# Optimization experiments

Hardware: AMD Instinct MI355X
Metric: run time of the kernel (lower is better)

Reference implementation:

```python
import jax, jax.numpy as jnp
import numpy as np

NUM_HEADS = 16
D_K = 8          # = n_wires in _QLayer
EMBED_DIM = NUM_HEADS * D_K
BATCH, SEQ = 8, 1024


def quantum_heads(x, theta):
    """Exact analytic simulation of the per-head 8-qubit circuit.

    Circuit per head vector v (len 8): RX(v_i) encoding on wire i, then
    trainable RX(theta_i) on wire i (RX angles add on |0>), then CNOT chain
    (0->1),(1->2),...,(6->7),(7->0), then <PauliZ> on every wire.

    Before the CNOTs each qubit is cos(a/2)|0> - i sin(a/2)|1> with
    a_i = v_i + theta_i, so bit_i ~ Bernoulli(sin^2(a_i/2)) independently and
    E[(-1)^{bit_i}] = cos(a_i). The CNOT chain is a permutation of basis
    states acting linearly over GF(2): output bit w is the XOR of input bits
    dep(w), where dep(0) = {1..7} and dep(w) = {0..w} for w>=1. Hence
    <Z_w> = prod_{j in dep(w)} cos(a_j).
    """
    b, s, e = x.shape
    a = x.reshape(b, s, NUM_HEADS, D_K) + theta      # [b,s,h,8]
    c = jnp.cos(a)
    cp = jnp.cumprod(c, axis=-1)                     # prefix products c0..cw
    z0 = jnp.prod(c[..., 1:], axis=-1, keepdims=True)  # wire 0: cos(a1)...cos(a7)
    z = jnp.concatenate([z0, cp[..., 1:]], axis=-1)  # [b,s,h,8]
    return z.reshape(b, s, e)


def setup_inputs() -> dict:
    key = jax.random.key(0)
    k1, k2, k3 = jax.random.split(key, 3)
    x = jax.random.normal(k1, (BATCH, SEQ, EMBED_DIM), dtype=jnp.float32)
    theta = jax.random.normal(k2, (D_K,), dtype=jnp.float32)
    w_combine = jax.random.normal(k3, (EMBED_DIM, EMBED_DIM), dtype=jnp.float32) * 0.05
    return {"x": x, "theta": theta, "w_combine": w_combine}


def reference(x, theta, w_combine):
    b, s, e = x.shape
    # The module calls the SAME _QLayer on the same x three times, so q=k=v.
    meas = quantum_heads(x, theta)                                   # [b,s,e]
    qkv = meas.reshape(b, s, NUM_HEADS, D_K).transpose(0, 2, 1, 3)   # [b,h,s,d]
    scores = jnp.einsum('bhqd,bhkd->bhqk', qkv, qkv) / np.float32(np.sqrt(D_K))
    attn = jax.nn.softmax(scores, axis=-1)
    out = jnp.einsum('bhqk,bhkd->bhqd', attn, qkv)
    out = out.transpose(0, 2, 1, 3).reshape(b, s, e)
    return out @ w_combine.T  # bias-free combine_heads Linear
```

## Files before the change

kernel.cpp:

```cpp
#include <hip/hip_runtime.h>
#include <hip/hip_bf16.h>

#define NUM_HEADS 16
#define EMBED 128
#define BATCH 8
#define SEQ 1024
#define ROWS (BATCH*SEQ)
#define QSCALE 0.5101256830f

#if __has_builtin(__builtin_amdgcn_exp2f)
#define EXP2(x) __builtin_amdgcn_exp2f(x)
#else
#define EXP2(x) exp2f(x)
#endif

__global__ __launch_bounds__(256) void k_wt(const float* __restrict__ w,
                                            float* __restrict__ wt) {
    int idx = blockIdx.x * 256 + threadIdx.x;
    int e = idx >> 7;
    int f = idx & 127;
    wt[f * 128 + e] = w[idx];
}

__global__ __launch_bounds__(256) void k_attn(const float* __restrict__ x,
                                              const float* __restrict__ theta,
                                              float* __restrict__ attn) {
    __shared__ __align__(16) float z[SEQ * 8];
    const int bid = blockIdx.x;
    const int bh = bid >> 1, qh = bid & 1;
    const int b = bh >> 4, h = bh & 15;
    const int t = threadIdx.x;

    float th[8];
#pragma unroll
    for (int i = 0; i < 8; ++i) th[i] = theta[i];

    float q[2][8];
#pragma unroll
    for (int j = 0; j < 4; ++j) {
        int r = t + 256 * j;
        const float* xp = x + ((size_t)((b << 10) + r)) * 128 + h * 8;
        float4 a0 = *(const float4*)xp;
        float4 a1 = *(const float4*)(xp + 4);
        float c0 = cosf(a0.x + th[0]);
        float c1 = cosf(a0.y + th[1]);
        float c2 = cosf(a0.z + th[2]);
        float c3 = cosf(a0.w + th[3]);
        float c4 = cosf(a1.x + th[4]);
        float c5 = cosf(a1.y + th[5]);
        float c6 = cosf(a1.z + th[6]);
        float c7 = cosf(a1.w + th[7]);
        float z1 = c0 * c1;
        float z2 = z1 * c2;
        float z3 = z2 * c3;
        float z4 = z3 * c4;
        float z5 = z4 * c5;
        float z6 = z5 * c6;
        float z7 = z6 * c7;
        float z0 = c1 * c2;
        z0 *= c3; z0 *= c4; z0 *= c5; z0 *= c6; z0 *= c7;
        *(float4*)&z[r * 8]     = make_float4(z0, z1, z2, z3);
        *(float4*)&z[r * 8 + 4] = make_float4(z4, z5, z6, z7);
        if ((j >> 1) == qh) {
            int jj = j & 1;
            q[jj][0] = z0 * QSCALE; q[jj][1] = z1 * QSCALE;
            q[jj][2] = z2 * QSCALE; q[jj][3] = z3 * QSCALE;
            q[jj][4] = z4 * QSCALE; q[jj][5] = z5 * QSCALE;
            q[jj][6] = z6 * QSCALE; q[jj][7] = z7 * QSCALE;
        }
    }
    __syncthreads();

    float o[2][8];
#pragma unroll
    for (int jj = 0; jj < 2; ++jj)
#pragma unroll
        for (int i = 0; i < 8; ++i) o[jj][i] = 0.f;
    float sm0 = 0.f, sm1 = 0.f;

#pragma unroll 4
    for (int kk = 0; kk < SEQ; ++kk) {
        float4 k0 = *(const float4*)&z[kk * 8];
        float4 k1 = *(const float4*)&z[kk * 8 + 4];
        float s0 = q[0][0]*k0.x + q[0][1]*k0.y + q[0][2]*k0.z + q[0][3]*k0.w
                 + q[0][4]*k1.x + q[0][5]*k1.y + q[0][6]*k1.z + q[0][7]*k1.w;
        float s1 = q[1][0]*k0.x + q[1][1]*k0.y + q[1][2]*k0.z + q[1][3]*k0.w
                 + q[1][4]*k1.x + q[1][5]*k1.y + q[1][6]*k1.z + q[1][7]*k1.w;
        float p0 = EXP2(s0);
        float p1 = EXP2(s1);
        sm0 += p0; sm1 += p1;
        o[0][0] += p0*k0.x; o[0][1] += p0*k0.y; o[0][2] += p0*k0.z; o[0][3] += p0*k0.w;
        o[0][4] += p0*k1.x; o[0][5] += p0*k1.y; o[0][6] += p0*k1.z; o[0][7] += p0*k1.w;
        o[1][0] += p1*k0.x; o[1][1] += p1*k0.y; o[1][2] += p1*k0.z; o[1][3] += p1*k0.w;
        o[1][4] += p1*k1.x; o[1][5] += p1*k1.y; o[1][6] += p1*k1.z; o[1][7] += p1*k1.w;
    }

    float inv0 = 1.0f / sm0;
    float inv1 = 1.0f / sm1;
    int r0 = qh * 512 + t;
    float* op = attn + ((size_t)((b << 10) + r0)) * 128 + h * 8;
    *(float4*)op       = make_float4(o[0][0]*inv0, o[0][1]*inv0, o[0][2]*inv0, o[0][3]*inv0);
    *(float4*)(op + 4) = make_float4(o[0][4]*inv0, o[0][5]*inv0, o[0][6]*inv0, o[0][7]*inv0);
    op += (size_t)256 * 128;
    *(float4*)op       = make_float4(o[1][0]*inv1, o[1][1]*inv1, o[1][2]*inv1, o[1][3]*inv1);
    *(float4*)(op + 4) = make_float4(o[1][4]*inv1, o[1][5]*inv1, o[1][6]*inv1, o[1][7]*inv1);
}

__global__ __launch_bounds__(256) void k_combine(const float* __restrict__ a,
                                                 const float* __restrict__ wt,
                                                 float* __restrict__ out) {
    int t = threadIdx.x;
    int e = t & 127;
    int half = t >> 7;
    size_t r0 = (size_t)blockIdx.x * 8 + half * 4;
    const float* arow = a + r0 * 128;

    float acc0 = 0.f, acc1 = 0.f, acc2 = 0.f, acc3 = 0.f;
#pragma unroll 4
    for (int f = 0; f < 128; ++f) {
        float wv = wt[f * 128 + e];
        acc0 += arow[f]       * wv;
        acc1 += arow[128 + f] * wv;
        acc2 += arow[256 + f] * wv;
        acc3 += arow[384 + f] * wv;
    }
    out[(r0 + 0) * 128 + e] = acc0;
    out[(r0 + 1) * 128 + e] = acc1;
    out[(r0 + 2) * 128 + e] = acc2;
    out[(r0 + 3) * 128 + e] = acc3;
}

extern "C" void kernel_launch(void* const* d_in, const int* in_sizes, int n_in,
                              void* d_out, int out_size, void* d_ws, size_t ws_size,
                              hipStream_t stream) {
    const float* x     = (const float*)d_in[0];
    const float* theta = (const float*)d_in[1];
    const float* w     = (const float*)d_in[2];
    float* out = (float*)d_out;

    float* attn = (float*)d_ws;
    float* wt   = (float*)((char*)d_ws + (size_t)ROWS * EMBED * 4);

    k_wt<<<64, 256, 0, stream>>>(w, wt);
    k_attn<<<256, 256, 0, stream>>>(x, theta, attn);
    k_combine<<<ROWS / 8, 256, 0, stream>>>(attn, wt, out);
}
```

Measured before the change: 165.3 us.

## Split attention queries across more blocks and stage combine rows in LDS

The attention kernel now launches 512 blocks, each handling 256 query rows with one query per thread instead of two. This doubles parallelism on the many-CU GPU, at the cost of recomputing the shared K/V (cosine products) in twice as many blocks. The combine kernel stages 16 activation rows in shared memory and computes 8 rows per thread with float4 LDS reads, reusing each weight load across more rows. It also adds FMA intrinsics, inline v_exp_f32 and launch-bounds occupancy hints.

```diff
diff --git a/kernel.cpp b/kernel.cpp
--- a/kernel.cpp
+++ b/kernel.cpp
@@ -8,11 +8,11 @@
 #define ROWS (BATCH*SEQ)
 #define QSCALE 0.5101256830f
 
-#if __has_builtin(__builtin_amdgcn_exp2f)
-#define EXP2(x) __builtin_amdgcn_exp2f(x)
-#else
-#define EXP2(x) exp2f(x)
-#endif
+__device__ __forceinline__ float fast_exp2(float x) {
+    float r;
+    asm("v_exp_f32 %0, %1" : "=v"(r) : "v"(x));
+    return r;
+}
 
 __global__ __launch_bounds__(256) void k_wt(const float* __restrict__ w,
                                             float* __restrict__ wt) {
@@ -22,12 +22,12 @@
     wt[f * 128 + e] = w[idx];
 }
 
-__global__ __launch_bounds__(256) void k_attn(const float* __restrict__ x,
-                                              const float* __restrict__ theta,
-                                              float* __restrict__ attn) {
+__global__ __launch_bounds__(256, 2) void k_attn(const float* __restrict__ x,
+                                                 const float* __restrict__ theta,
+                                                 float* __restrict__ attn) {
     __shared__ __align__(16) float z[SEQ * 8];
     const int bid = blockIdx.x;
-    const int bh = bid >> 1, qh = bid & 1;
+    const int bh = bid >> 2, qc = bid & 3;
     const int b = bh >> 4, h = bh & 15;
     const int t = threadIdx.x;
 
@@ -35,7 +35,7 @@
 #pragma unroll
     for (int i = 0; i < 8; ++i) th[i] = theta[i];
 
-    float q[2][8];
+    float q[8];
 #pragma unroll
     for (int j = 0; j < 4; ++j) {
         int r = t + 256 * j;
@@ -61,73 +61,88 @@
         z0 *= c3; z0 *= c4; z0 *= c5; z0 *= c6; z0 *= c7;
         *(float4*)&z[r * 8]     = make_float4(z0, z1, z2, z3);
         *(float4*)&z[r * 8 + 4] = make_float4(z4, z5, z6, z7);
-        if ((j >> 1) == qh) {
-            int jj = j & 1;
-            q[jj][0] = z0 * QSCALE; q[jj][1] = z1 * QSCALE;
-            q[jj][2] = z2 * QSCALE; q[jj][3] = z3 * QSCALE;
-            q[jj][4] = z4 * QSCALE; q[jj][5] = z5 * QSCALE;
-            q[jj][6] = z6 * QSCALE; q[jj][7] = z7 * QSCALE;
+        if (j == qc) {
+            q[0] = z0 * QSCALE; q[1] = z1 * QSCALE;
+            q[2] = z2 * QSCALE; q[3] = z3 * QSCALE;
+            q[4] = z4 * QSCALE; q[5] = z5 * QSCALE;
+            q[6] = z6 * QSCALE; q[7] = z7 * QSCALE;
         }
     }
     __syncthreads();
 
-    float o[2][8];
-#pragma unroll
-    for (int jj = 0; jj < 2; ++jj)
-#pragma unroll
-        for (int i = 0; i < 8; ++i) o[jj][i] = 0.f;
-    float sm0 = 0.f, sm1 = 0.f;
+    float o0 = 0.f, o1 = 0.f, o2 = 0.f, o3 = 0.f;
+    float o4 = 0.f, o5 = 0.f, o6 = 0.f, o7 = 0.f;
+    float sm = 0.f;
 
 #pragma unroll 4
     for (int kk = 0; kk < SEQ; ++kk) {
         float4 k0 = *(const float4*)&z[kk * 8];
         float4 k1 = *(const float4*)&z[kk * 8 + 4];
-        float s0 = q[0][0]*k0.x + q[0][1]*k0.y + q[0][2]*k0.z + q[0][3]*k0.w
-                 + q[0][4]*k1.x + q[0][5]*k1.y + q[0][6]*k1.z + q[0][7]*k1.w;
-        float s1 = q[1][0]*k0.x + q[1][1]*k0.y + q[1][2]*k0.z + q[1][3]*k0.w
-                 + q[1][4]*k1.x + q[1][5]*k1.y + q[1][6]*k1.z + q[1][7]*k1.w;
-        float p0 = EXP2(s0);
-        float p1 = EXP2(s1);
-        sm0 += p0; sm1 += p1;
-        o[0][0] += p0*k0.x; o[0][1] += p0*k0.y; o[0][2] += p0*k0.z; o[0][3] += p0*k0.w;
-        o[0][4] += p0*k1.x; o[0][5] += p0*k1.y; o[0][6] += p0*k1.z; o[0][7] += p0*k1.w;
-        o[1][0] += p1*k0.x; o[1][1] += p1*k0.y; o[1][2] += p1*k0.z; o[1][3] += p1*k0.w;
-        o[1][4] += p1*k1.x; o[1][5] += p1*k1.y; o[1][6] += p1*k1.z; o[1][7] += p1*k1.w;
+        float sa = __builtin_fmaf(q[0], k0.x,
+                   __builtin_fmaf(q[1], k0.y,
+                   __builtin_fmaf(q[2], k0.z, q[3] * k0.w)));
+        float sb = __builtin_fmaf(q[4], k1.x,
+                   __builtin_fmaf(q[5], k1.y,
+                   __builtin_fmaf(q[6], k1.z, q[7] * k1.w)));
+        float p = fast_exp2(sa + sb);
+        sm += p;
+        o0 = __builtin_fmaf(p, k0.x, o0);
+        o1 = __builtin_fmaf(p, k0.y, o1);
+        o2 = __builtin_fmaf(p, k0.z, o2);
+        o3 = __builtin_fmaf(p, k0.w, o3);
+        o4 = __builtin_fmaf(p, k1.x, o4);
+        o5 = __builtin_fmaf(p, k1.y, o5);
+        o6 = __builtin_fmaf(p, k1.z, o6);
+        o7 = __builtin_fmaf(p, k1.w, o7);
     }
 
-    float inv0 = 1.0f / sm0;
-    float inv1 = 1.0f / sm1;
-    int r0 = qh * 512 + t;
+    float inv = 1.0f / sm;
+    int r0 = qc * 256 + t;
     float* op = attn + ((size_t)((b << 10) + r0)) * 128 + h * 8;
-    *(float4*)op       = make_float4(o[0][0]*inv0, o[0][1]*inv0, o[0][2]*inv0, o[0][3]*inv0);
-    *(float4*)(op + 4) = make_float4(o[0][4]*inv0, o[0][5]*inv0, o[0][6]*inv0, o[0][7]*inv0);
-    op += (size_t)256 * 128;
-    *(float4*)op       = make_float4(o[1][0]*inv1, o[1][1]*inv1, o[1][2]*inv1, o[1][3]*inv1);
-    *(float4*)(op + 4) = make_float4(o[1][4]*inv1, o[1][5]*inv1, o[1][6]*inv1, o[1][7]*inv1);
+    *(float4*)op       = make_float4(o0 * inv, o1 * inv, o2 * inv, o3 * inv);
+    *(float4*)(op + 4) = make_float4(o4 * inv, o5 * inv, o6 * inv, o7 * inv);
 }
 
-__global__ __launch_bounds__(256) void k_combine(const float* __restrict__ a,
-                                                 const float* __restrict__ wt,
-                                                 float* __restrict__ out) {
+__global__ __launch_bounds__(256, 2) void k_combine(const float* __restrict__ a,
+                                                    const float* __restrict__ wt,
+                                                    float* __restrict__ out) {
+    __shared__ __align__(16) float at[16 * 128];
     int t = threadIdx.x;
+    size_t r0 = (size_t)blockIdx.x * 16;
+
+    const float4* asrc = (const float4*)(a + r0 * 128);
+    float4* adst = (float4*)at;
+    adst[t]       = asrc[t];
+    adst[t + 256] = asrc[t + 256];
+    __syncthreads();
+
     int e = t & 127;
-    int half = t >> 7;
-    size_t r0 = (size_t)blockIdx.x * 8 + half * 4;
-    const float* arow = a + r0 * 128;
+    int rg = (t >> 7) * 8;
 
-    float acc0 = 0.f, acc1 = 0.f, acc2 = 0.f, acc3 = 0.f;
-#pragma unroll 4
-    for (int f = 0; f < 128; ++f) {
-        float wv = wt[f * 128 + e];
-        acc0 += arow[f]       * wv;
-        acc1 += arow[128 + f] * wv;
-        acc2 += arow[256 + f] * wv;
-        acc3 += arow[384 + f] * wv;
+    float acc[8];
+#pragma unroll
+    for (int r = 0; r < 8; ++r) acc[r] = 0.f;
+
+#pragma unroll 8
+    for (int f4 = 0; f4 < 32; ++f4) {
+        int f = f4 * 4;
+        float w0 = wt[(f + 0) * 128 + e];
+        float w1 = wt[(f + 1) * 128 + e];
+        float w2 = wt[(f + 2) * 128 + e];
+        float w3 = wt[(f + 3) * 128 + e];
+#pragma unroll
+        for (int r = 0; r < 8; ++r) {
+            float4 av = *(const float4*)&at[(rg + r) * 128 + f];
+            acc[r] = __builtin_fmaf(av.x, w0, acc[r]);
+            acc[r] = __builtin_fmaf(av.y, w1, acc[r]);
+            acc[r] = __builtin_fmaf(av.z, w2, acc[r]);
+            acc[r] = __builtin_fmaf(av.w, w3, acc[r]);
+        }
     }
-    out[(r0 + 0) * 128 + e] = acc0;
-    out[(r0 + 1) * 128 + e] = acc1;
-    out[(r0 + 2) * 128 + e] = acc2;
-    out[(r0 + 3) * 128 + e] = acc3;
+
+#pragma unroll
+    for (int r = 0; r < 8; ++r)
+        out[(r0 + rg + r) * 128 + e] = acc[r];
 }
 
 extern "C" void kernel_launch(void* const* d_in, const int* in_sizes, int n_in,
@@ -142,6 +157,6 @@
     float* wt   = (float*)((char*)d_ws + (size_t)ROWS * EMBED * 4);
 
     k_wt<<<64, 256, 0, stream>>>(w, wt);
-    k_attn<<<256, 256, 0, stream>>>(x, theta, attn);
-    k_combine<<<ROWS / 8, 256, 0, stream>>>(attn, wt, out);
+    k_attn<<<512, 256, 0, stream>>>(x, theta, attn);
+    k_combine<<<ROWS / 16, 256, 0, stream>>>(attn, wt, out);
 }
```

New measurement: 158.6 us. -4.0%, faster.
